# Performance work log

Measured on AMD Instinct MI355X. Metric: run time of the kernel, lower is better.

## Reference

```python
import math
import jax, jax.numpy as jnp
import numpy as np
from jax import lax

W_DIM = 512
UP = 2
K = 3
LRELU_GAIN = math.sqrt(2.0)  # bias_act def_gain for 'lrelu'
CLAMP = 256.0                # conv_clamp * gain(=1)


def setup_inputs() -> dict:
    key = jax.random.key(0)
    ks = jax.random.split(key, 8)
    B, Cin, Cout, H = 16, 512, 512, 32
    return {
        "x": jax.random.normal(ks[0], (B, Cin, H, H), jnp.float32),
        "w_latent": jax.random.normal(ks[1], (B, W_DIM), jnp.float32),
        "affine_weight": jax.random.normal(ks[2], (Cin, W_DIM), jnp.float32),
        "affine_bias": jnp.ones((Cin,), jnp.float32),  # bias_init=1
        "conv_weight": jax.random.normal(ks[3], (Cout, Cin, K, K), jnp.float32),
        "noise": jax.random.normal(ks[4], (B, 1, 2 * H, 2 * H), jnp.float32),
        "noise_strength": jax.random.uniform(ks[5], (1,), jnp.float32),
        "bias": jax.random.normal(ks[6], (Cout,), jnp.float32),
    }


def reference(x, w_latent, affine_weight, affine_bias, conv_weight, noise, noise_strength, bias):
    B, Cin, H, W = x.shape
    Cout = conv_weight.shape[0]

    # EqualFullyConnectedLayer (linear act): style = w @ (W * 1/sqrt(in)).T + b
    style = w_latent @ (affine_weight * (1.0 / math.sqrt(W_DIM))).T + affine_bias  # [B, Cin]

    # Modulate + demodulate per-sample weights: [B, Cout, Cin, K, K]
    wmod = conv_weight[None] * style[:, None, :, None, None]
    dcoefs = lax.rsqrt(jnp.sum(wmod * wmod, axis=(2, 3, 4)) + 1e-8)  # [B, Cout]
    wmod = wmod * dcoefs[:, :, None, None, None]

    # Grouped transposed conv (stride=UP), batch-as-groups trick.
    # torch.conv_transpose2d(x, w.transpose, stride=UP) == dilated conv with
    # spatially-flipped modulated weight, lhs_dilation=UP, padding=K-1.
    w_eff = wmod.reshape(B * Cout, Cin, K, K)[:, :, ::-1, ::-1]
    x1 = x.reshape(1, B * Cin, H, W)
    y = lax.conv_general_dilated(
        x1, w_eff, window_strides=(1, 1),
        padding=[(K - 1, K - 1), (K - 1, K - 1)],
        lhs_dilation=(UP, UP), feature_group_count=B,
        dimension_numbers=("NCHW", "OIHW", "NCHW"))  # [1, B*Cout, 2H+1, 2W+1]

    # upfirdn2d: FIR low-pass (1,3,3,1) outer, normalized, gain=up^2, pad (1,1,1,1)
    f1 = jnp.array([1.0, 3.0, 3.0, 1.0], jnp.float32)
    f2 = jnp.outer(f1, f1)
    f2 = f2 / f2.sum() * (UP * UP)
    yc = y.reshape(B * Cout, 1, 2 * H + 1, 2 * W + 1)
    y = lax.conv_general_dilated(
        yc, f2[None, None], window_strides=(1, 1), padding=[(1, 1), (1, 1)],
        dimension_numbers=("NCHW", "OIHW", "NCHW"))
    y = y.reshape(B, Cout, 2 * H, 2 * W)

    # noise injection + fused bias + lrelu(gain=sqrt(2)) + clamp
    y = y + noise * noise_strength[0]
    y = y + bias[None, :, None, None]
    y = jax.nn.leaky_relu(y, negative_slope=0.2) * LRELU_GAIN
    return jnp.clip(y, -CLAMP, CLAMP)
```

## Files before the change

### kernel.cpp

```cpp
#include <hip/hip_runtime.h>
#include <hip/hip_bf16.h>


typedef unsigned short u16;
typedef unsigned int u32;
typedef u16 u16x8 __attribute__((ext_vector_type(8)));
typedef __bf16 bf16x8 __attribute__((ext_vector_type(8)));
typedef float f32x4 __attribute__((ext_vector_type(4)));

#define NB 16

__device__ __forceinline__ float bf2f(u16 v) {
  unsigned int u = ((unsigned int)v) << 16;
  float f;
  __builtin_memcpy(&f, &u, 4);
  return f;
}
__device__ __forceinline__ u16 f2bf(float f) {
  __hip_bfloat16 h = __float2bfloat16(f);
  u16 r;
  __builtin_memcpy(&r, &h, 2);
  return r;
}
__device__ __forceinline__ void async16(u16* lds, const u16* g) {
  __builtin_amdgcn_global_load_lds(
      (const __attribute__((address_space(1))) u32*)g,
      (__attribute__((address_space(3))) u32*)lds, 16, 0, 0);
}

__global__ __launch_bounds__(256) void k_style(const float* __restrict__ wl,
                                               const float* __restrict__ aw,
                                               const float* __restrict__ ab,
                                               float* __restrict__ style) {
  __shared__ float lw[512];
  const int b = blockIdx.y;
  const int c = blockIdx.x * 256 + threadIdx.x;
  for (int k = threadIdx.x; k < 512; k += 256) lw[k] = wl[b * 512 + k];
  __syncthreads();
  const float* row = aw + (size_t)c * 512;
  float acc = 0.f;
#pragma unroll 8
  for (int k = 0; k < 512; ++k) acc += lw[k] * row[k];
  style[b * 512 + c] = acc * 0.04419417382415922f + ab[c];
}

__global__ __launch_bounds__(256) void k_wprep(const float* __restrict__ cw,
                                               const float* __restrict__ style,
                                               float* __restrict__ dcoef,
                                               u16* __restrict__ W2) {
  __shared__ u16 lw[4608];
  __shared__ float wsq[512];
  const int o = blockIdx.x, t = threadIdx.x;
  const float* src = cw + (size_t)o * 4608;
  for (int v = t; v < 4608; v += 256) {
    unsigned c = (unsigned)v / 9u;
    unsigned kp = (unsigned)v % 9u;
    lw[kp * 512 + c] = f2bf(src[v]);
  }
  for (int c = t; c < 512; c += 256) {
    const float* p = src + (size_t)c * 9;
    float s = 0.f;
#pragma unroll
    for (int k = 0; k < 9; ++k) {
      float v = p[k];
      s += v * v;
    }
    wsq[c] = s;
  }
  __syncthreads();
  u16* dst = W2 + (size_t)o * 4608;
  for (int v = t; v < 576; v += 256)
    *(u16x8*)(dst + v * 8) = *(const u16x8*)(lw + v * 8);
  const int w = t >> 6, l = t & 63;
  for (int b = w; b < NB; b += 4) {
    float part = 0.f;
#pragma unroll
    for (int c = l; c < 512; c += 64) {
      float st = style[b * 512 + c];
      part += st * st * wsq[c];
    }
#pragma unroll
    for (int off = 32; off; off >>= 1) part += __shfl_down(part, off, 64);
    if (l == 0) dcoef[b * 512 + o] = 1.0f / sqrtf(part + 1e-8f);
  }
}

__global__ __launch_bounds__(256) void k_xt(const float* __restrict__ x,
                                            const float* __restrict__ style,
                                            u16* __restrict__ xT) {
  __shared__ u16 tile[64 * 66];
  const int b = blockIdx.z, c0 = blockIdx.y << 6, s0 = blockIdx.x << 6;
  const int t = threadIdx.x;
#pragma unroll
  for (int i = 0; i < 16; ++i) {
    int e = i * 256 + t;
    int cc = e >> 6, ss = e & 63;
    int c = c0 + cc;
    float v = x[(size_t)(b * 512 + c) * 1024 + s0 + ss] * style[b * 512 + c];
    tile[cc * 66 + ss] = f2bf(v);
  }
  __syncthreads();
#pragma unroll
  for (int e = 0; e < 2; ++e) {
    int idx = e * 256 + t;
    int sc = idx >> 3;
    int cg = (idx & 7) << 3;
    u16x8 v;
#pragma unroll
    for (int g = 0; g < 8; ++g) v[g] = tile[(cg + g) * 66 + sc];
    *(u16x8*)(xT + (size_t)(b * 1024 + s0 + sc) * 512 + c0 + cg) = v;
  }
}

__global__ __launch_bounds__(256) void k_gemm(const u16* __restrict__ W2,
                                              const u16* __restrict__ xT,
                                              u16* __restrict__ Z) {
  __shared__ u16 At[128 * 32];
  __shared__ u16 Bt[128 * 32];
  const int t = threadIdx.x;
  const int m0 = blockIdx.y << 7;
  const int n0 = blockIdx.x << 7;
  const int l = t & 63;
  const int w = t >> 6;
  const int wy = ((t >> 7) & 1) << 6;
  const int wx = ((t >> 6) & 1) << 6;
  const int lrow = l & 15;

  const int sr = t >> 2;
  const int sch = ((t & 3) + (sr >> 1)) & 3;
  const u16* gA = W2 + (size_t)(m0 + sr) * 512 + (sch << 3);
  const u16* gB = xT + (size_t)(n0 + sr) * 512 + (sch << 3);
  u16* lA0 = At + (w << 9);
  u16* lA1 = At + 2048 + (w << 9);
  u16* lB0 = Bt + (w << 9);
  u16* lB1 = Bt + 2048 + (w << 9);

  const int sk8 = (((l >> 4) - (lrow >> 1)) & 3) << 3;

  f32x4 acc[4][4] = {};

  for (int k0 = 0; k0 < 512; k0 += 32) {
    async16(lA0, gA + k0);
    async16(lA1, gA + k0 + 64 * 512);
    async16(lB0, gB + k0);
    async16(lB1, gB + k0 + 64 * 512);
    asm volatile("s_waitcnt vmcnt(0)" ::: "memory");
    __syncthreads();
    bf16x8 av[4], bv[4];
#pragma unroll
    for (int i = 0; i < 4; ++i)
      av[i] = *(const bf16x8*)(At + (wy + i * 16 + lrow) * 32 + sk8);
#pragma unroll
    for (int j = 0; j < 4; ++j)
      bv[j] = *(const bf16x8*)(Bt + (wx + j * 16 + lrow) * 32 + sk8);
#pragma unroll
    for (int i = 0; i < 4; ++i)
#pragma unroll
      for (int j = 0; j < 4; ++j)
        acc[i][j] = __builtin_amdgcn_mfma_f32_16x16x32_bf16(av[i], bv[j], acc[i][j], 0, 0, 0);
    __syncthreads();
  }

  const int mr = m0 + wy + ((l >> 4) << 2);
  const int nc = n0 + wx + lrow;
#pragma unroll
  for (int i = 0; i < 4; ++i)
#pragma unroll
    for (int j = 0; j < 4; ++j)
#pragma unroll
      for (int r = 0; r < 4; ++r)
        Z[(size_t)(mr + i * 16 + r) * 16384 + nc + j * 16] = f2bf(acc[i][j][r]);
}

__global__ __launch_bounds__(256) void k_scatter(
    const u16* __restrict__ Z, const float* __restrict__ dcoef,
    const float* __restrict__ noise, const float* __restrict__ nstr,
    const float* __restrict__ bias, float* __restrict__ out) {
  __shared__ u16 Zl[9 * 1024];
  __shared__ float Hl[3 * 2048];
  const int o = blockIdx.x;
  const int b = blockIdx.y;
  const int t = threadIdx.x;
  const u16* Zp = Z + (size_t)o * 9 * 16384 + (size_t)b * 1024;
  for (int v = t; v < 1152; v += 256) {
    int kp = v >> 7, off = (v & 127) << 3;
    *(u16x8*)(Zl + kp * 1024 + off) = *(const u16x8*)(Zp + (size_t)kp * 16384 + off);
  }
  __syncthreads();
#pragma unroll
  for (int e = 0; e < 12; ++e) {
    int idx = e * 256 + t;
    int ky = idx >> 10;
    int i = (idx >> 5) & 31;
    int j = idx & 31;
    const u16* P0 = Zl + (ky * 3 + 0) * 1024 + i * 32;
    const u16* P1 = P0 + 1024;
    const u16* P2 = P0 + 2048;
    float Ej = bf2f(P0[j]) + (j >= 1 ? bf2f(P2[j - 1]) : 0.f);
    float Ej1 = (j < 31 ? bf2f(P0[j + 1]) : 0.f) + bf2f(P2[j]);
    float Ojm = j >= 1 ? bf2f(P1[j - 1]) : 0.f;
    float Oj = bf2f(P1[j]);
    float Ojp = j < 31 ? bf2f(P1[j + 1]) : 0.f;
    float* hp = Hl + ky * 2048 + i * 64 + j;
    hp[0] = Ojm + 3.f * Ej + 3.f * Oj + Ej1;
    hp[32] = Ej + 3.f * Oj + 3.f * Ej1 + Ojp;
  }
  __syncthreads();
  const float dc = dcoef[b * 512 + o] * 0.0625f;
  const float ns = nstr[0];
  const float bo = bias[o];
  const int n = t & 63;
  const int i0 = (t >> 6) << 3;
  const int sw = ((n & 1) << 5) | (n >> 1);
  const float* H0 = Hl + sw;
  const float* H1 = Hl + 2048 + sw;
  const float* H2 = Hl + 4096 + sw;
  float h0 = H0[i0 * 64];
  float h1 = H1[i0 * 64];
  float h1p = (i0 > 0) ? H1[(i0 - 1) * 64] : 0.f;
  float h2p = (i0 > 0) ? H2[(i0 - 1) * 64] : 0.f;
  const float* nz = noise + ((size_t)b << 12) + n;
  float* op = out + (((size_t)(b * 512 + o)) << 12) + n;
#pragma unroll
  for (int s = 0; s < 8; ++s) {
    int i = i0 + s;
    float h0n = (i < 31) ? H0[(i + 1) * 64] : 0.f;
    float h1n = (i < 31) ? H1[(i + 1) * 64] : 0.f;
    float h2 = H2[i * 64];
    float ev = h1p + 3.f * (h0 + h2p) + 3.f * h1 + (h0n + h2);
    float od = (h0 + h2p) + 3.f * h1 + 3.f * (h0n + h2) + h1n;
    int m = 2 * i;
    float v0 = ev * dc + nz[(size_t)m * 64] * ns + bo;
    v0 = (v0 > 0.f ? v0 : 0.2f * v0) * 1.4142135623730951f;
    v0 = fminf(fmaxf(v0, -256.f), 256.f);
    op[(size_t)m * 64] = v0;
    float v1 = od * dc + nz[(size_t)(m + 1) * 64] * ns + bo;
    v1 = (v1 > 0.f ? v1 : 0.2f * v1) * 1.4142135623730951f;
    v1 = fminf(fmaxf(v1, -256.f), 256.f);
    op[(size_t)(m + 1) * 64] = v1;
    h0 = h0n;
    h1p = h1;
    h1 = h1n;
    h2p = h2;
  }
}

extern "C" void kernel_launch(void* const* d_in, const int* in_sizes, int n_in,
                              void* d_out, int out_size, void* d_ws, size_t ws_size,
                              hipStream_t stream) {
  const float* x = (const float*)d_in[0];
  const float* wl = (const float*)d_in[1];
  const float* aw = (const float*)d_in[2];
  const float* ab = (const float*)d_in[3];
  const float* cw = (const float*)d_in[4];
  const float* noise = (const float*)d_in[5];
  const float* nstr = (const float*)d_in[6];
  const float* bias = (const float*)d_in[7];
  float* out = (float*)d_out;

  float* style = (float*)d_ws;
  float* dcoef = style + 8192;
  u16* W2 = (u16*)(dcoef + 8192);
  u16* xT = W2 + 4608 * 512;
  u16* Z = xT + (size_t)16384 * 512;

  k_style<<<dim3(2, 16), 256, 0, stream>>>(wl, aw, ab, style);
  k_wprep<<<dim3(512), 256, 0, stream>>>(cw, style, dcoef, W2);
  k_xt<<<dim3(16, 8, 16), 256, 0, stream>>>(x, style, xT);
  k_gemm<<<dim3(128, 36), 256, 0, stream>>>(W2, xT, Z);
  k_scatter<<<dim3(512, 16), 256, 0, stream>>>(Z, dcoef, noise, nstr, bias, out);
}
```

Before: 377.5 us.

## Enlarge GEMM tile to 256x256 with 4-stage async LDS pipeline

Rewrites the bf16 GEMM to use 512-thread blocks computing 256x256 tiles, with a 4-buffer LDS ring that prefetches two k-steps ahead. Loads for the next stages are interleaved between two MFMA phases, gated by vmcnt waits, s_barrier and setprio. The goal is to hide global-load latency behind MFMA work and to reuse more data per LDS fetch. In exchange it uses much more LDS (128KB per block) and more registers, and launch_bounds(512,2) may not hold given that LDS size.

```diff
diff --git a/kernel.cpp b/kernel.cpp
--- a/kernel.cpp
+++ b/kernel.cpp
@@ -112,59 +112,102 @@
   }
 }
 
-__global__ __launch_bounds__(256) void k_gemm(const u16* __restrict__ W2,
-                                              const u16* __restrict__ xT,
-                                              u16* __restrict__ Z) {
-  __shared__ u16 At[128 * 32];
-  __shared__ u16 Bt[128 * 32];
+__global__ __launch_bounds__(512, 2) void k_gemm(const u16* __restrict__ W2,
+                                                 const u16* __restrict__ xT,
+                                                 u16* __restrict__ Z) {
+  __shared__ u16 At[4][8192];
+  __shared__ u16 Bt[4][8192];
   const int t = threadIdx.x;
-  const int m0 = blockIdx.y << 7;
-  const int n0 = blockIdx.x << 7;
+  const int m0 = blockIdx.y << 8;
+  const int n0 = blockIdx.x << 8;
   const int l = t & 63;
   const int w = t >> 6;
-  const int wy = ((t >> 7) & 1) << 6;
-  const int wx = ((t >> 6) & 1) << 6;
+  const int wm = w >> 2;
+  const int wn = w & 3;
   const int lrow = l & 15;
+  const int lk = l >> 4;
 
   const int sr = t >> 2;
   const int sch = ((t & 3) + (sr >> 1)) & 3;
   const u16* gA = W2 + (size_t)(m0 + sr) * 512 + (sch << 3);
   const u16* gB = xT + (size_t)(n0 + sr) * 512 + (sch << 3);
-  u16* lA0 = At + (w << 9);
-  u16* lA1 = At + 2048 + (w << 9);
-  u16* lB0 = Bt + (w << 9);
-  u16* lB1 = Bt + 2048 + (w << 9);
-
-  const int sk8 = (((l >> 4) - (lrow >> 1)) & 3) << 3;
-
-  f32x4 acc[4][4] = {};
-
-  for (int k0 = 0; k0 < 512; k0 += 32) {
-    async16(lA0, gA + k0);
-    async16(lA1, gA + k0 + 64 * 512);
-    async16(lB0, gB + k0);
-    async16(lB1, gB + k0 + 64 * 512);
-    asm volatile("s_waitcnt vmcnt(0)" ::: "memory");
-    __syncthreads();
-    bf16x8 av[4], bv[4];
+  const int wb = w << 9;
+
+  const int sk8 = ((lk - (lrow >> 1)) & 3) << 3;
+  const int arow = (wm << 7) + lrow;
+  const int brow = (wn << 6) + lrow;
+
+  f32x4 acc[8][4] = {};
+
+#define STAGE_A(nb_, kt_)                                   \
+  async16(&At[nb_][wb], gA + (kt_) * 32);                   \
+  async16(&At[nb_][4096 + wb], gA + (kt_) * 32 + 65536)
+#define STAGE_B(nb_, kt_)                                   \
+  async16(&Bt[nb_][wb], gB + (kt_) * 32);                   \
+  async16(&Bt[nb_][4096 + wb], gB + (kt_) * 32 + 65536)
+
+  STAGE_A(0, 0);
+  STAGE_B(0, 0);
+  STAGE_A(1, 1);
+  STAGE_B(1, 1);
+  asm volatile("s_waitcnt vmcnt(4)" ::: "memory");
+  asm volatile("s_barrier" ::: "memory");
+
+  for (int kt = 0; kt < 16; ++kt) {
+    const int buf = kt & 3;
+    const int nb = (kt + 2) & 3;
+    const u16* Ab = At[buf];
+    const u16* Bb = Bt[buf];
+    bf16x8 av[4], bv[4], av2[4];
+
 #pragma unroll
     for (int i = 0; i < 4; ++i)
-      av[i] = *(const bf16x8*)(At + (wy + i * 16 + lrow) * 32 + sk8);
+      av[i] = *(const bf16x8*)(Ab + (arow + i * 16) * 32 + sk8);
 #pragma unroll
     for (int j = 0; j < 4; ++j)
-      bv[j] = *(const bf16x8*)(Bt + (wx + j * 16 + lrow) * 32 + sk8);
+      bv[j] = *(const bf16x8*)(Bb + (brow + j * 16) * 32 + sk8);
+    if (kt < 14) { STAGE_A(nb, kt + 2); }
+    asm volatile("s_barrier" ::: "memory");
+    asm volatile("s_waitcnt lgkmcnt(0)" ::: "memory");
+    __builtin_amdgcn_sched_barrier(0);
+    __builtin_amdgcn_s_setprio(1);
 #pragma unroll
     for (int i = 0; i < 4; ++i)
 #pragma unroll
       for (int j = 0; j < 4; ++j)
         acc[i][j] = __builtin_amdgcn_mfma_f32_16x16x32_bf16(av[i], bv[j], acc[i][j], 0, 0, 0);
-    __syncthreads();
-  }
-
-  const int mr = m0 + wy + ((l >> 4) << 2);
-  const int nc = n0 + wx + lrow;
-#pragma unroll
-  for (int i = 0; i < 4; ++i)
+    __builtin_amdgcn_s_setprio(0);
+    asm volatile("s_barrier" ::: "memory");
+
+#pragma unroll
+    for (int i = 0; i < 4; ++i)
+      av2[i] = *(const bf16x8*)(Ab + (arow + 64 + i * 16) * 32 + sk8);
+    if (kt < 14) { STAGE_B(nb, kt + 2); }
+    asm volatile("s_barrier" ::: "memory");
+    asm volatile("s_waitcnt lgkmcnt(0)" ::: "memory");
+    __builtin_amdgcn_sched_barrier(0);
+    __builtin_amdgcn_s_setprio(1);
+#pragma unroll
+    for (int i = 0; i < 4; ++i)
+#pragma unroll
+      for (int j = 0; j < 4; ++j)
+        acc[i + 4][j] = __builtin_amdgcn_mfma_f32_16x16x32_bf16(av2[i], bv[j], acc[i + 4][j], 0, 0, 0);
+    __builtin_amdgcn_s_setprio(0);
+
+    if (kt < 14) {
+      asm volatile("s_waitcnt vmcnt(4)" ::: "memory");
+    } else if (kt == 14) {
+      asm volatile("s_waitcnt vmcnt(0)" ::: "memory");
+    }
+    asm volatile("s_barrier" ::: "memory");
+  }
+#undef STAGE_A
+#undef STAGE_B
+
+  const int mr = m0 + (wm << 7) + (lk << 2);
+  const int nc = n0 + (wn << 6) + lrow;
+#pragma unroll
+  for (int i = 0; i < 8; ++i)
 #pragma unroll
     for (int j = 0; j < 4; ++j)
 #pragma unroll
@@ -267,6 +310,6 @@
   k_style<<<dim3(2, 16), 256, 0, stream>>>(wl, aw, ab, style);
   k_wprep<<<dim3(512), 256, 0, stream>>>(cw, style, dcoef, W2);
   k_xt<<<dim3(16, 8, 16), 256, 0, stream>>>(x, style, xT);
-  k_gemm<<<dim3(128, 36), 256, 0, stream>>>(W2, xT, Z);
+  k_gemm<<<dim3(64, 18), 512, 0, stream>>>(W2, xT, Z);
   k_scatter<<<dim3(512, 16), 256, 0, stream>>>(Z, dcoef, noise, nstr, bias, out);
 }
```

Result: no change. 382.6 us (+1.4%).
